# Kernel tuning notes

Measured on AMD Instinct MI355X. Metric: run time of the kernel, lower is better.

Reference implementation:

```python
import jax, jax.numpy as jnp
import numpy as np

B, S, D, H = 2, 2048, 1024, 16
DH = D // H  # 64

def setup_inputs() -> dict:
    key = jax.random.key(0)
    ks = jax.random.split(key, 10)
    sc = 1.0 / np.sqrt(D)
    x = jax.random.normal(ks[0], (B, S, D), dtype=jnp.float32)
    Wq = jax.random.normal(ks[1], (H, D, DH), dtype=jnp.float32) * sc
    bq = jax.random.normal(ks[2], (H, DH), dtype=jnp.float32) * 0.01
    Wk = jax.random.normal(ks[3], (H, D, DH), dtype=jnp.float32) * sc
    bk = jax.random.normal(ks[4], (H, DH), dtype=jnp.float32) * 0.01
    Wv = jax.random.normal(ks[5], (H, D, DH), dtype=jnp.float32) * sc
    bv = jax.random.normal(ks[6], (H, DH), dtype=jnp.float32) * 0.01
    Wo = jax.random.normal(ks[7], (H * DH, D), dtype=jnp.float32) * sc
    bo = jax.random.normal(ks[8], (D,), dtype=jnp.float32) * 0.01
    return {"x": x, "Wq": Wq, "bq": bq, "Wk": Wk, "bk": bk, "Wv": Wv, "bv": bv, "Wo": Wo, "bo": bo}

def reference(x, Wq, bq, Wk, bk, Wv, bv, Wo, bo):
    # Batched per-head QKV projections (original loops over heads with small Linears)
    q = jnp.einsum('bsd,hde->bhse', x, Wq) + bq[None, :, None, :]  # [B,H,S,DH]
    k = jnp.einsum('bsd,hde->bhse', x, Wk) + bk[None, :, None, :]
    v = jnp.einsum('bsd,hde->bhse', x, Wv) + bv[None, :, None, :]
    scores = jnp.einsum('bhse,bhte->bhst', q, k) / jnp.sqrt(jnp.asarray(DH, q.dtype))
    probs = jax.nn.softmax(scores, axis=-1)  # dropout p=0 (eval)
    ctx = jnp.einsum('bhst,bhte->bhse', probs, v)  # [B,H,S,DH]
    # concat heads along feature dim (head order matches torch.cat over heads)
    ctx = jnp.transpose(ctx, (0, 2, 1, 3)).reshape(B, S, H * DH)
    out = ctx @ Wo + bo  # output projection, dropout p=0
    return out
```

## Files before the change

kernel.cpp:

```cpp
#include <hip/hip_runtime.h>
#include <hip/hip_bf16.h>


constexpr int B  = 2;
constexpr int S  = 2048;
constexpr int D  = 1024;
constexpr int H  = 16;
constexpr int DH = 64;
constexpr int BS = B * S;

using u16 = unsigned short;
using u32 = unsigned int;
using frag8  = __attribute__((ext_vector_type(8)))  short;
using f32x4  = __attribute__((ext_vector_type(4)))  float;
using f32x16 = __attribute__((ext_vector_type(16))) float;

__device__ inline u16 f2bf(float x) {
    u32 u = __float_as_uint(x);
    return (u16)((u + 0x7FFF + ((u >> 16) & 1)) >> 16);
}
__device__ inline u32 pk2(float a, float b) {
    __hip_bfloat162 t = __float22bfloat162_rn(make_float2(a, b));
    union { __hip_bfloat162 h; u32 u; } c; c.h = t; return c.u;
}
__device__ inline float unpk_lo(u32 p) { return __uint_as_float(p << 16); }
__device__ inline float unpk_hi(u32 p) { return __uint_as_float(p & 0xffff0000u); }

__device__ inline void glds16(const u16* g, const u16* l) {
    __builtin_amdgcn_global_load_lds(
        (const __attribute__((address_space(1))) void*)g,
        (__attribute__((address_space(3))) void*)l, 16, 0, 0);
}

#define KSC (0.125f * 1.44269504088896f)

__global__ __launch_bounds__(256) void convert_x(
    const float* __restrict__ x, u16* __restrict__ xh, u16* __restrict__ xl)
{
    const size_t idx = ((size_t)blockIdx.x * 256 + threadIdx.x) * 4;
    float4 v = *(const float4*)&x[idx];
    u32 h01 = pk2(v.x, v.y), h23 = pk2(v.z, v.w);
    *(uint2*)&xh[idx] = make_uint2(h01, h23);
    *(uint2*)&xl[idx] = make_uint2(pk2(v.x - unpk_lo(h01), v.y - unpk_hi(h01)),
                                   pk2(v.z - unpk_lo(h23), v.w - unpk_hi(h23)));
}

__global__ __launch_bounds__(256) void transpose_w(
    const float* __restrict__ Wq, const float* __restrict__ Wk,
    const float* __restrict__ Wv, const float* __restrict__ Wo,
    u16* __restrict__ Wt)
{
    const int kt = blockIdx.x;
    const int sl = blockIdx.y;
    const int tid = threadIdx.x;
    __shared__ float Ls[64][68];

    const float* src; int rstride;
    if (sl < 48) {
        const int t = sl >> 4, h = sl & 15;
        const float* Wp = (t == 0) ? Wq : ((t == 1) ? Wk : Wv);
        src = Wp + (size_t)h * D * DH;
        rstride = 64;
    } else {
        src = Wo + (sl - 48) * 64;
        rstride = 1024;
    }

    const int rr = tid >> 4, c4 = tid & 15;
#pragma unroll
    for (int p = 0; p < 4; ++p) {
        const int kk = p * 16 + rr;
        float4 v = *(const float4*)&src[(size_t)(kt * 64 + kk) * rstride + c4 * 4];
        *(float4*)&Ls[kk][c4 * 4] = v;
    }
    __syncthreads();
    const int rl = tid >> 2, ks = tid & 3;
    u16 ob[16];
#pragma unroll
    for (int i = 0; i < 16; ++i) ob[i] = f2bf(Ls[ks * 16 + i][rl]);
    u16* dst = Wt + (size_t)(sl * 64 + rl) * 1024 + kt * 64 + ks * 16;
    *(uint4*)&dst[0] = *(uint4*)&ob[0];
    *(uint4*)&dst[8] = *(uint4*)&ob[8];
}

__global__ __launch_bounds__(256, 3) void gemm_qkv(
    const u16* __restrict__ Wt, const u16* __restrict__ xh, const u16* __restrict__ xl,
    const float* __restrict__ bq, const float* __restrict__ bk, const float* __restrict__ bv,
    u16* __restrict__ qhO, u16* __restrict__ khF, u16* __restrict__ vhF)
{
    const int r0  = blockIdx.x * 128;
    const int c0  = blockIdx.y * 128;
    const int tid = threadIdx.x;
    const int w = tid >> 6, lane = tid & 63;
    const int wi = w >> 1, wj = w & 1;
    const int ml = lane & 15, kg = lane >> 4;

    __shared__ u16 Ta[2][128 * 32];
    __shared__ u16 Tb[2][128 * 32];
    __shared__ u16 Tl[2][128 * 32];

    const int srow = lane >> 2, sseg = lane & 3;
    const u16* Ag = Wt + (size_t)(r0 + w * 32 + srow) * 1024 + sseg * 8;
    const u16* Bg = xh + (size_t)(c0 + w * 32 + srow) * 1024 + sseg * 8;
    const u16* Lg = xl + (size_t)(c0 + w * 32 + srow) * 1024 + sseg * 8;

    f32x4 acc[4][4];
#pragma unroll
    for (int i = 0; i < 4; ++i)
#pragma unroll
        for (int j = 0; j < 4; ++j)
#pragma unroll
            for (int r = 0; r < 4; ++r) acc[i][j][r] = 0.f;

    for (int k0 = 0; k0 < 1024; k0 += 64) {
        __syncthreads();
#pragma unroll
        for (int hb = 0; hb < 2; ++hb) {
            const int ko = k0 + hb * 32;
            glds16(Ag + ko,             &Ta[hb][(w * 32) * 32]);
            glds16(Ag + 16 * 1024 + ko, &Ta[hb][(w * 32 + 16) * 32]);
            glds16(Bg + ko,             &Tb[hb][(w * 32) * 32]);
            glds16(Bg + 16 * 1024 + ko, &Tb[hb][(w * 32 + 16) * 32]);
            glds16(Lg + ko,             &Tl[hb][(w * 32) * 32]);
            glds16(Lg + 16 * 1024 + ko, &Tl[hb][(w * 32 + 16) * 32]);
        }
        __syncthreads();

#pragma unroll
        for (int hb = 0; hb < 2; ++hb) {
            frag8 af[4], bf[4], lf[4];
#pragma unroll
            for (int i = 0; i < 4; ++i)
                af[i] = *(const frag8*)&Ta[hb][(wi * 64 + i * 16 + ml) * 32 + kg * 8];
#pragma unroll
            for (int j = 0; j < 4; ++j) {
                bf[j] = *(const frag8*)&Tb[hb][(wj * 64 + j * 16 + ml) * 32 + kg * 8];
                lf[j] = *(const frag8*)&Tl[hb][(wj * 64 + j * 16 + ml) * 32 + kg * 8];
            }
#pragma unroll
            for (int i = 0; i < 4; ++i)
#pragma unroll
                for (int j = 0; j < 4; ++j) {
                    acc[i][j] = __builtin_amdgcn_mfma_f32_16x16x32_bf16(af[i], bf[j], acc[i][j], 0, 0, 0);
                    acc[i][j] = __builtin_amdgcn_mfma_f32_16x16x32_bf16(af[i], lf[j], acc[i][j], 0, 0, 0);
                }
        }
    }

    const int t = r0 >> 10;
    if (t == 0) {
#pragma unroll
        for (int i = 0; i < 4; ++i) {
            const int Rb = r0 + wi * 64 + i * 16 + kg * 4;
            const int h  = (Rb >> 6) & 15;
            const int e0 = Rb & 63;
            float bv4[4];
#pragma unroll
            for (int r = 0; r < 4; ++r) bv4[r] = bq[(Rb & 1023) + r];
#pragma unroll
            for (int j = 0; j < 4; ++j) {
                const int s  = c0 + wj * 64 + j * 16 + ml;
                const int bb = s >> 11, sl = s & (S - 1);
                float v[4];
#pragma unroll
                for (int r = 0; r < 4; ++r) v[r] = acc[i][j][r] + bv4[r];
                const size_t base = ((size_t)(bb * H + h) * S + sl) * 64 + e0;
                *(uint2*)&qhO[base] = make_uint2(pk2(v[0], v[1]), pk2(v[2], v[3]));
            }
        }
    } else if (t == 1) {
#pragma unroll
        for (int i = 0; i < 4; ++i) {
            const int Rb = r0 + wi * 64 + i * 16 + kg * 4;
            const int h  = (Rb >> 6) & 15;
            const int e0 = Rb & 63;
            const int ksf = e0 >> 4, Hf = (e0 >> 3) & 1, j0 = e0 & 7;
            float bv4[4];
#pragma unroll
            for (int r = 0; r < 4; ++r) bv4[r] = bk[(Rb & 1023) + r];
#pragma unroll
            for (int j = 0; j < 4; ++j) {
                const int s  = c0 + wj * 64 + j * 16 + ml;
                const int bb = s >> 11, sl = s & (S - 1);
                const int bh = bb * H + h;
                const int kt = sl >> 6, sub = (sl >> 5) & 1, klow = sl & 31;
                const int lanef = klow | (Hf << 5);
                const size_t off = (size_t)bh * 131072 +
                    (size_t)(((kt * 2 + sub) * 4 + ksf) * 64 + lanef) * 8 + j0;
                float v[4];
#pragma unroll
                for (int r = 0; r < 4; ++r) v[r] = (acc[i][j][r] + bv4[r]) * KSC;
                *(uint2*)&khF[off] = make_uint2(pk2(v[0], v[1]), pk2(v[2], v[3]));
            }
        }
    } else {
#pragma unroll
        for (int i = 0; i < 4; ++i) {
            const int Rb  = r0 + wi * 64 + i * 16 + kg * 4;
            const int h   = (Rb >> 6) & 15;
            const int dh0 = Rb & 63;
            float bv4[4];
#pragma unroll
            for (int r = 0; r < 4; ++r) bv4[r] = bv[(Rb & 1023) + r];
#pragma unroll
            for (int j = 0; j < 4; ++j) {
                const int s  = c0 + wj * 64 + j * 16 + ml;
                const int bb = s >> 11, sl = s & (S - 1);
                const int bh = bb * H + h;
                const int kt = sl >> 6, key = sl & 63;
                const int ksf = key >> 4, Hf = (key >> 3) & 1, j0 = key & 7;
                const size_t tb = (size_t)bh * 131072 + (size_t)j0 +
                                  (size_t)((kt * 2) * 4 + ksf) * 512;
#pragma unroll
                for (int r = 0; r < 4; ++r) {
                    const int dh = dh0 + r;
                    const int sub = dh >> 5;
                    const int lanef = (dh & 31) | (Hf << 5);
                    vhF[tb + (size_t)sub * 2048 + (size_t)lanef * 8] =
                        f2bf(acc[i][j][r] + bv4[r]);
                }
            }
        }
    }
}

__global__ __launch_bounds__(512, 4) void attention_mfma(
    const u16* __restrict__ qh, const u16* __restrict__ khF,
    const u16* __restrict__ vhF,
    u16* __restrict__ cth, u16* __restrict__ ctl)
{
    const int id  = blockIdx.x;
    const int bh  = (id & 7) | (((id >> 3) & 3) << 3);
    const int qt  = id >> 5;
    const int b   = bh >> 4, h = bh & 15;
    const int tid = threadIdx.x;
    const int w   = tid >> 6, wl = w & 3, g = w >> 2;
    const int lane = tid & 63;
    const int nq  = lane & 31;
    const int Hh  = lane >> 5;

    __shared__ union {
        u16   stg[2][2][2][4096];
        float xch[128][72];
    } L;
    __shared__ float lsum[2][128];

    const int qrow = qt * 128 + wl * 32 + nq;
    const u16* qhp = qh + ((size_t)bh * S + qrow) * DH;
    frag8 qf[4];
#pragma unroll
    for (int ks = 0; ks < 4; ++ks) qf[ks] = *(const frag8*)(qhp + ks * 16 + Hh * 8);

    f32x16 O0, O1;
#pragma unroll
    for (int i = 0; i < 16; ++i) { O0[i] = 0.f; O1[i] = 0.f; }
    float l_run = 0.f;

    const int go = wl * 1024 + lane * 8;
    const size_t bhb = (size_t)bh * 131072;

    {
        const size_t kb = bhb + (size_t)(g * 16) * 4096;
        glds16(khF + kb + go,       &L.stg[g][0][0][wl * 1024]);
        glds16(khF + kb + go + 512, &L.stg[g][0][0][wl * 1024 + 512]);
        glds16(vhF + kb + go,       &L.stg[g][0][1][wl * 1024]);
        glds16(vhF + kb + go + 512, &L.stg[g][0][1][wl * 1024 + 512]);
    }

    for (int it = 0; it < 16; ++it) {
        __syncthreads();
        if (it < 15) {
            const size_t kb = bhb + (size_t)(g * 16 + it + 1) * 4096;
            const int nb = (it + 1) & 1;
            glds16(khF + kb + go,       &L.stg[g][nb][0][wl * 1024]);
            glds16(khF + kb + go + 512, &L.stg[g][nb][0][wl * 1024 + 512]);
            glds16(vhF + kb + go,       &L.stg[g][nb][1][wl * 1024]);
            glds16(vhF + kb + go + 512, &L.stg[g][nb][1][wl * 1024 + 512]);
        }
        const u16* sK = &L.stg[g][it & 1][0][0];
        const u16* sV = &L.stg[g][it & 1][1][0];

        f32x16 sa0, sa1;
#pragma unroll
        for (int i = 0; i < 16; ++i) { sa0[i] = 0.f; sa1[i] = 0.f; }
#pragma unroll
        for (int ks = 0; ks < 4; ++ks) {
            frag8 k0 = *(const frag8*)&sK[(ks * 64 + lane) * 8];
            frag8 k1 = *(const frag8*)&sK[((4 + ks) * 64 + lane) * 8];
            sa0 = __builtin_amdgcn_mfma_f32_32x32x16_bf16(k0, qf[ks], sa0, 0, 0, 0);
            sa1 = __builtin_amdgcn_mfma_f32_32x32x16_bf16(k1, qf[ks], sa1, 0, 0, 0);
        }

        float psum = 0.f;
        u32 ph0[8], ph1[8];
#pragma unroll
        for (int u = 0; u < 8; ++u) {
            float e0 = exp2f(sa0[2 * u]);
            float e1 = exp2f(sa0[2 * u + 1]);
            float f0 = exp2f(sa1[2 * u]);
            float f1 = exp2f(sa1[2 * u + 1]);
            psum += (e0 + e1) + (f0 + f1);
            ph0[u] = pk2(e0, e1);
            ph1[u] = pk2(f0, f1);
        }
        l_run += psum;

#pragma unroll
        for (int ks = 0; ks < 4; ++ks) {
            const u32* PH = (ks < 2) ? ph0 : ph1;
            const int ks2 = ks & 1;
            const int oi = 4 * ks2 + 2 * Hh;
            const int si = 4 * ks2 + 2 * (1 - Hh);
            u32 rh0 = __shfl_xor(PH[si], 32), rh1 = __shfl_xor(PH[si + 1], 32);
            union { u32 u[4]; frag8 f; } fh;
            if (Hh == 0) {
                fh.u[0] = PH[oi]; fh.u[1] = PH[oi + 1]; fh.u[2] = rh0; fh.u[3] = rh1;
            } else {
                fh.u[0] = rh0; fh.u[1] = rh1; fh.u[2] = PH[oi]; fh.u[3] = PH[oi + 1];
            }
            frag8 v0 = *(const frag8*)&sV[(ks * 64 + lane) * 8];
            frag8 v1 = *(const frag8*)&sV[((4 + ks) * 64 + lane) * 8];
            O0 = __builtin_amdgcn_mfma_f32_32x32x16_bf16(v0, fh.f, O0, 0, 0, 0);
            O1 = __builtin_amdgcn_mfma_f32_32x32x16_bf16(v1, fh.f, O1, 0, 0, 0);
        }
    }

    l_run += __shfl_xor(l_run, 32);
    const int qr = wl * 32 + nq;
    if (Hh == 0) lsum[g][qr] = l_run;
    __syncthreads();
    const float invl = 1.f / (lsum[0][qr] + lsum[1][qr]);

    if (g == 1) {
#pragma unroll
        for (int cdh = 0; cdh < 2; ++cdh)
#pragma unroll
            for (int rg = 0; rg < 4; ++rg) {
                const f32x16& O = cdh ? O1 : O0;
                float4 v4;
                v4.x = O[4 * rg + 0]; v4.y = O[4 * rg + 1];
                v4.z = O[4 * rg + 2]; v4.w = O[4 * rg + 3];
                *(float4*)&L.xch[qr][cdh * 32 + rg * 8 + Hh * 4] = v4;
            }
    }
    __syncthreads();
    if (g == 0) {
#pragma unroll
        for (int cdh = 0; cdh < 2; ++cdh)
#pragma unroll
            for (int rg = 0; rg < 4; ++rg) {
                float4 p4 = *(const float4*)&L.xch[qr][cdh * 32 + rg * 8 + Hh * 4];
                const f32x16& O = cdh ? O1 : O0;
                float4 v4;
                v4.x = (O[4 * rg + 0] + p4.x) * invl;
                v4.y = (O[4 * rg + 1] + p4.y) * invl;
                v4.z = (O[4 * rg + 2] + p4.z) * invl;
                v4.w = (O[4 * rg + 3] + p4.w) * invl;
                *(float4*)&L.xch[qr][cdh * 32 + rg * 8 + Hh * 4] = v4;
            }
    }
    __syncthreads();
#pragma unroll
    for (int pass = 0; pass < 4; ++pass) {
        const int chunk = pass * 512 + tid;
        const int qi = chunk >> 4, seg = chunk & 15;
        float4 v4 = *(const float4*)&L.xch[qi][seg * 4];
        u32 h01 = pk2(v4.x, v4.y), h23 = pk2(v4.z, v4.w);
        const size_t base = ((size_t)(b * S + qt * 128 + qi)) * D + h * DH + seg * 4;
        *(uint2*)&cth[base] = make_uint2(h01, h23);
        *(uint2*)&ctl[base] = make_uint2(pk2(v4.x - unpk_lo(h01), v4.y - unpk_hi(h01)),
                                         pk2(v4.z - unpk_lo(h23), v4.w - unpk_hi(h23)));
    }
}

__global__ __launch_bounds__(256, 4) void gemm_out(
    const u16* __restrict__ Ah, const u16* __restrict__ Al,
    const u16* __restrict__ Bh, const float* __restrict__ bo,
    float* __restrict__ out)
{
    const int r0  = blockIdx.x * 128;
    const int c0  = blockIdx.y * 64;
    const int tid = threadIdx.x;
    const int w = tid >> 6, lane = tid & 63;
    const int ml = lane & 15, kg = lane >> 4;

    __shared__ u16 Ta[2][128 * 32];
    __shared__ u16 Tl[2][128 * 32];
    __shared__ u16 Tb[2][64 * 32];

    const int srow = lane >> 2, sseg = lane & 3;
    const u16* Ag = Ah + (size_t)(r0 + w * 32 + srow) * 1024 + sseg * 8;
    const u16* Lg = Al + (size_t)(r0 + w * 32 + srow) * 1024 + sseg * 8;
    const u16* Bg = Bh + (size_t)(c0 + w * 16 + srow) * 1024 + sseg * 8;

    f32x4 acc[2][4];
#pragma unroll
    for (int i = 0; i < 2; ++i)
#pragma unroll
        for (int j = 0; j < 4; ++j)
#pragma unroll
            for (int r = 0; r < 4; ++r) acc[i][j][r] = 0.f;

    for (int k0 = 0; k0 < 1024; k0 += 64) {
        __syncthreads();
#pragma unroll
        for (int hb = 0; hb < 2; ++hb) {
            const int ko = k0 + hb * 32;
            glds16(Ag + ko,             &Ta[hb][(w * 32) * 32]);
            glds16(Ag + 16 * 1024 + ko, &Ta[hb][(w * 32 + 16) * 32]);
            glds16(Lg + ko,             &Tl[hb][(w * 32) * 32]);
            glds16(Lg + 16 * 1024 + ko, &Tl[hb][(w * 32 + 16) * 32]);
            glds16(Bg + ko,             &Tb[hb][(w * 16) * 32]);
        }
        __syncthreads();

#pragma unroll
        for (int hb = 0; hb < 2; ++hb) {
            frag8 af[2], lf[2], bf[4];
#pragma unroll
            for (int i = 0; i < 2; ++i) {
                af[i] = *(const frag8*)&Ta[hb][(w * 32 + i * 16 + ml) * 32 + kg * 8];
                lf[i] = *(const frag8*)&Tl[hb][(w * 32 + i * 16 + ml) * 32 + kg * 8];
            }
#pragma unroll
            for (int j = 0; j < 4; ++j)
                bf[j] = *(const frag8*)&Tb[hb][(j * 16 + ml) * 32 + kg * 8];
#pragma unroll
            for (int i = 0; i < 2; ++i)
#pragma unroll
                for (int j = 0; j < 4; ++j) {
                    acc[i][j] = __builtin_amdgcn_mfma_f32_16x16x32_bf16(af[i], bf[j], acc[i][j], 0, 0, 0);
                    acc[i][j] = __builtin_amdgcn_mfma_f32_16x16x32_bf16(lf[i], bf[j], acc[i][j], 0, 0, 0);
                }
        }
    }

#pragma unroll
    for (int i = 0; i < 2; ++i) {
        const int R0 = r0 + w * 32 + i * 16 + kg * 4;
#pragma unroll
        for (int j = 0; j < 4; ++j) {
            const int col = c0 + j * 16 + ml;
            const float bval = bo[col];
#pragma unroll
            for (int r = 0; r < 4; ++r)
                out[(size_t)(R0 + r) * 1024 + col] = acc[i][j][r] + bval;
        }
    }
}

extern "C" void kernel_launch(void* const* d_in, const int* in_sizes, int n_in,
                              void* d_out, int out_size, void* d_ws, size_t ws_size,
                              hipStream_t stream) {
    (void)in_sizes; (void)n_in; (void)out_size; (void)ws_size;
    const float* x  = (const float*)d_in[0];
    const float* Wq = (const float*)d_in[1];
    const float* bq = (const float*)d_in[2];
    const float* Wk = (const float*)d_in[3];
    const float* bk = (const float*)d_in[4];
    const float* Wv = (const float*)d_in[5];
    const float* bv = (const float*)d_in[6];
    const float* Wo = (const float*)d_in[7];
    const float* bo = (const float*)d_in[8];
    float* out = (float*)d_out;

    const size_t NPER = (size_t)BS * D;
    u16* base = (u16*)d_ws;
    u16* xh  = base;
    u16* xl  = base + NPER;
    u16* Wt  = base + 2 * NPER;
    u16* qh  = base + 3 * NPER;
    u16* khF = base + 4 * NPER;
    u16* vhF = base + 5 * NPER;
    u16* cth = xh;
    u16* ctl = xl;

    convert_x  <<<dim3(BS * D / 1024), 256, 0, stream>>>(x, xh, xl);
    transpose_w<<<dim3(16, 64),        256, 0, stream>>>(Wq, Wk, Wv, Wo, Wt);
    gemm_qkv   <<<dim3(24, 32), 256, 0, stream>>>(Wt, xh, xl, bq, bk, bv,
                                                  qh, khF, vhF);
    attention_mfma<<<dim3(512), 512, 0, stream>>>(qh, khF, vhF, cth, ctl);
    gemm_out   <<<dim3(32, 16), 256, 0, stream>>>(cth, ctl, Wt + (size_t)3072 * 1024,
                                                  bo, out);
}
```

Before: 259.1 us.

## Load K/V fragments directly from global into registers, drop LDS staging

The attention kernel stops staging K and V tiles through double-buffered shared memory with async global-to-LDS loads and per-iteration block barriers. Each wave now reads its MFMA fragments straight from global memory into registers, since the pre-swizzled layout makes them contiguous. exp2f is also swapped for the hardware exp2 builtin. This removes the __syncthreads inside the loop and the LDS round trip, but the four waves sharing a K/V group now fetch the same data redundantly through cache. Without explicit prefetch, global load latency is also exposed right before each MFMA chain.

```diff
diff --git a/kernel.cpp b/kernel.cpp
--- a/kernel.cpp
+++ b/kernel.cpp
@@ -25,6 +25,12 @@
 }
 __device__ inline float unpk_lo(u32 p) { return __uint_as_float(p << 16); }
 __device__ inline float unpk_hi(u32 p) { return __uint_as_float(p & 0xffff0000u); }
+
+#if __has_builtin(__builtin_amdgcn_exp2f)
+#define EXP2(x) __builtin_amdgcn_exp2f(x)
+#else
+#define EXP2(x) exp2f(x)
+#endif
 
 __device__ inline void glds16(const u16* g, const u16* l) {
     __builtin_amdgcn_global_load_lds(
@@ -239,10 +245,7 @@
     const int nq  = lane & 31;
     const int Hh  = lane >> 5;
 
-    __shared__ union {
-        u16   stg[2][2][2][4096];
-        float xch[128][72];
-    } L;
+    __shared__ float xch[128][72];
     __shared__ float lsum[2][128];
 
     const int qrow = qt * 128 + wl * 32 + nq;
@@ -256,49 +259,39 @@
     for (int i = 0; i < 16; ++i) { O0[i] = 0.f; O1[i] = 0.f; }
     float l_run = 0.f;
 
-    const int go = wl * 1024 + lane * 8;
-    const size_t bhb = (size_t)bh * 131072;
-
-    {
-        const size_t kb = bhb + (size_t)(g * 16) * 4096;
-        glds16(khF + kb + go,       &L.stg[g][0][0][wl * 1024]);
-        glds16(khF + kb + go + 512, &L.stg[g][0][0][wl * 1024 + 512]);
-        glds16(vhF + kb + go,       &L.stg[g][0][1][wl * 1024]);
-        glds16(vhF + kb + go + 512, &L.stg[g][0][1][wl * 1024 + 512]);
-    }
+    const size_t gbase = (size_t)bh * 131072 + (size_t)(g * 16) * 4096 + (size_t)lane * 8;
+    const u16* kB = khF + gbase;
+    const u16* vB = vhF + gbase;
 
     for (int it = 0; it < 16; ++it) {
-        __syncthreads();
-        if (it < 15) {
-            const size_t kb = bhb + (size_t)(g * 16 + it + 1) * 4096;
-            const int nb = (it + 1) & 1;
-            glds16(khF + kb + go,       &L.stg[g][nb][0][wl * 1024]);
-            glds16(khF + kb + go + 512, &L.stg[g][nb][0][wl * 1024 + 512]);
-            glds16(vhF + kb + go,       &L.stg[g][nb][1][wl * 1024]);
-            glds16(vhF + kb + go + 512, &L.stg[g][nb][1][wl * 1024 + 512]);
-        }
-        const u16* sK = &L.stg[g][it & 1][0][0];
-        const u16* sV = &L.stg[g][it & 1][1][0];
+        const u16* kT = kB + (size_t)it * 4096;
+        const u16* vT = vB + (size_t)it * 4096;
+
+        frag8 kf[8];
+#pragma unroll
+        for (int p = 0; p < 8; ++p) kf[p] = *(const frag8*)&kT[p * 512];
 
         f32x16 sa0, sa1;
 #pragma unroll
         for (int i = 0; i < 16; ++i) { sa0[i] = 0.f; sa1[i] = 0.f; }
 #pragma unroll
         for (int ks = 0; ks < 4; ++ks) {
-            frag8 k0 = *(const frag8*)&sK[(ks * 64 + lane) * 8];
-            frag8 k1 = *(const frag8*)&sK[((4 + ks) * 64 + lane) * 8];
-            sa0 = __builtin_amdgcn_mfma_f32_32x32x16_bf16(k0, qf[ks], sa0, 0, 0, 0);
-            sa1 = __builtin_amdgcn_mfma_f32_32x32x16_bf16(k1, qf[ks], sa1, 0, 0, 0);
-        }
+            sa0 = __builtin_amdgcn_mfma_f32_32x32x16_bf16(kf[ks],     qf[ks], sa0, 0, 0, 0);
+            sa1 = __builtin_amdgcn_mfma_f32_32x32x16_bf16(kf[4 + ks], qf[ks], sa1, 0, 0, 0);
+        }
+
+        frag8 vf[8];
+#pragma unroll
+        for (int p = 0; p < 8; ++p) vf[p] = *(const frag8*)&vT[p * 512];
 
         float psum = 0.f;
         u32 ph0[8], ph1[8];
 #pragma unroll
         for (int u = 0; u < 8; ++u) {
-            float e0 = exp2f(sa0[2 * u]);
-            float e1 = exp2f(sa0[2 * u + 1]);
-            float f0 = exp2f(sa1[2 * u]);
-            float f1 = exp2f(sa1[2 * u + 1]);
+            float e0 = EXP2(sa0[2 * u]);
+            float e1 = EXP2(sa0[2 * u + 1]);
+            float f0 = EXP2(sa1[2 * u]);
+            float f1 = EXP2(sa1[2 * u + 1]);
             psum += (e0 + e1) + (f0 + f1);
             ph0[u] = pk2(e0, e1);
             ph1[u] = pk2(f0, f1);
@@ -318,8 +311,8 @@
             } else {
                 fh.u[0] = rh0; fh.u[1] = rh1; fh.u[2] = PH[oi]; fh.u[3] = PH[oi + 1];
             }
-            frag8 v0 = *(const frag8*)&sV[(ks * 64 + lane) * 8];
-            frag8 v1 = *(const frag8*)&sV[((4 + ks) * 64 + lane) * 8];
+            frag8 v0 = vf[ks];
+            frag8 v1 = vf[4 + ks];
             O0 = __builtin_amdgcn_mfma_f32_32x32x16_bf16(v0, fh.f, O0, 0, 0, 0);
             O1 = __builtin_amdgcn_mfma_f32_32x32x16_bf16(v1, fh.f, O1, 0, 0, 0);
         }
@@ -340,7 +333,7 @@
                 float4 v4;
                 v4.x = O[4 * rg + 0]; v4.y = O[4 * rg + 1];
                 v4.z = O[4 * rg + 2]; v4.w = O[4 * rg + 3];
-                *(float4*)&L.xch[qr][cdh * 32 + rg * 8 + Hh * 4] = v4;
+                *(float4*)&xch[qr][cdh * 32 + rg * 8 + Hh * 4] = v4;
             }
     }
     __syncthreads();
@@ -349,14 +342,14 @@
         for (int cdh = 0; cdh < 2; ++cdh)
 #pragma unroll
             for (int rg = 0; rg < 4; ++rg) {
-                float4 p4 = *(const float4*)&L.xch[qr][cdh * 32 + rg * 8 + Hh * 4];
+                float4 p4 = *(const float4*)&xch[qr][cdh * 32 + rg * 8 + Hh * 4];
                 const f32x16& O = cdh ? O1 : O0;
                 float4 v4;
                 v4.x = (O[4 * rg + 0] + p4.x) * invl;
                 v4.y = (O[4 * rg + 1] + p4.y) * invl;
                 v4.z = (O[4 * rg + 2] + p4.z) * invl;
                 v4.w = (O[4 * rg + 3] + p4.w) * invl;
-                *(float4*)&L.xch[qr][cdh * 32 + rg * 8 + Hh * 4] = v4;
+                *(float4*)&xch[qr][cdh * 32 + rg * 8 + Hh * 4] = v4;
             }
     }
     __syncthreads();
@@ -364,7 +357,7 @@
     for (int pass = 0; pass < 4; ++pass) {
         const int chunk = pass * 512 + tid;
         const int qi = chunk >> 4, seg = chunk & 15;
-        float4 v4 = *(const float4*)&L.xch[qi][seg * 4];
+        float4 v4 = *(const float4*)&xch[qi][seg * 4];
         u32 h01 = pk2(v4.x, v4.y), h23 = pk2(v4.z, v4.w);
         const size_t base = ((size_t)(b * S + qt * 128 + qi)) * D + h * DH + seg * 4;
         *(uint2*)&cth[base] = make_uint2(h01, h23);
```

After: 278.1 us. 1.07x slower.
